# Kernel tuning notes

Measured on AMD Instinct MI355X. Metric: run time of the kernel, lower is better.

Reference implementation:

```python
import jax, jax.numpy as jnp
import numpy as np

B, C, H, W = 2, 512, 32, 32
HEADS = 8      # attention heads
GROUPS = 8     # offset groups (defaults to heads)
DH = 64        # dim_head
DF = 4         # downsample_factor
OFF_SCALE = 4.0
EPS = 1e-5


def _bn(t, gamma, beta):
    # eval-mode BatchNorm2d with running_mean=0, running_var=1
    s = gamma / jnp.sqrt(1.0 + EPS)
    return t * s[None, :, None, None] + beta[None, :, None, None]


def _gconv1x1(t, w):
    # grouped 1x1 conv (bias-free); w: (GROUPS, out_per_group, in_per_group)
    b, c, h, ww = t.shape
    o = jnp.einsum('bgci,goc->bgoi', t.reshape(b, GROUPS, c // GROUPS, h * ww), w)
    return o.reshape(b, GROUPS * w.shape[1], h, ww)


def _grid_sample(img, grid):
    # F.grid_sample: bilinear, padding_mode='zeros', align_corners=False
    # img: (N,Ci,Hi,Wi); grid: (N,Hg,Wg,2), grid[...,0]=x, grid[...,1]=y in [-1,1]
    N, Ci, Hi, Wi = img.shape
    gx = (grid[..., 0] + 1.0) * (Wi / 2.0) - 0.5
    gy = (grid[..., 1] + 1.0) * (Hi / 2.0) - 0.5
    x0 = jnp.floor(gx)
    y0 = jnp.floor(gy)
    wx = gx - x0
    wy = gy - y0

    def gather(im, ix, iy):
        valid = (ix >= 0) & (ix < Wi) & (iy >= 0) & (iy < Hi)
        ixc = jnp.clip(ix, 0, Wi - 1).astype(jnp.int32)
        iyc = jnp.clip(iy, 0, Hi - 1).astype(jnp.int32)
        return im[:, iyc, ixc] * valid[None].astype(im.dtype)

    def sample_one(im, x0, y0, wx, wy):
        v00 = gather(im, x0, y0)
        v01 = gather(im, x0 + 1, y0)
        v10 = gather(im, x0, y0 + 1)
        v11 = gather(im, x0 + 1, y0 + 1)
        wx = wx[None]
        wy = wy[None]
        return (v00 * (1 - wx) * (1 - wy) + v01 * wx * (1 - wy)
                + v10 * (1 - wx) * wy + v11 * wx * wy)

    return jax.vmap(sample_one)(img, x0, y0, wx, wy)


def _forward(x, bn1_g, bn1_b, bn2_g, bn2_b, qw, kw, vw, out_w, out_b,
             off_dw_w, off_dw_b, off_pw_w,
             cpb_w1, cpb_b1, cpb_w2, cpb_b2, cpb_w3, cpb_b3,
             mlp_w1, mlp_b1, mlp_w2, mlp_b2):
    b = x.shape[0]
    xn = _bn(x, bn1_g, bn1_b)
    # ---- deformable attention ----
    q = _gconv1x1(xn, qw)                                   # (b, 512, H, W)
    qg = q.reshape(b * GROUPS, DH, H, W)
    # to_offsets: depthwise conv k=6, s=4, p=1 -> GELU -> 1x1(64->2) -> tanh * offset_scale
    off = jax.lax.conv_general_dilated(
        qg, off_dw_w, (DF, DF), ((1, 1), (1, 1)),
        dimension_numbers=('NCHW', 'OIHW', 'NCHW'), feature_group_count=DH)
    off = jax.nn.gelu(off + off_dw_b[None, :, None, None], approximate=False)
    off = jnp.tanh(jnp.einsum('bchw,oc->bohw', off, off_pw_w)) * OFF_SCALE   # (b*G, 2, Hd, Wd)
    Hd, Wd = off.shape[-2], off.shape[-1]
    gy, gx = jnp.meshgrid(jnp.arange(Hd, dtype=x.dtype), jnp.arange(Wd, dtype=x.dtype), indexing='ij')
    vx = gx[None] + off[:, 0]
    vy = gy[None] + off[:, 1]
    # normalize_grid (lucidrains): first comp by (Hd-1), second by (Wd-1)
    nx = 2.0 * vx / max(Hd - 1, 1) - 1.0
    ny = 2.0 * vy / max(Wd - 1, 1) - 1.0
    vgrid_scaled = jnp.stack((nx, ny), axis=-1)             # (b*G, Hd, Wd, 2)
    kv = _grid_sample(xn.reshape(b * GROUPS, DH, H, W), vgrid_scaled)
    kv = kv.reshape(b, GROUPS * DH, Hd, Wd)
    k = _gconv1x1(kv, kw)
    v = _gconv1x1(kv, vw)
    scale = DH ** -0.5
    qh = q.reshape(b, HEADS, DH, H * W).transpose(0, 1, 3, 2) * scale    # (b,h,i,d)
    kh = k.reshape(b, HEADS, DH, Hd * Wd).transpose(0, 1, 3, 2)          # (b,h,j,d)
    vh = v.reshape(b, HEADS, DH, Hd * Wd).transpose(0, 1, 3, 2)
    # continuous relative position bias (CPB)
    qgy, qgx = jnp.meshgrid(jnp.arange(H, dtype=x.dtype), jnp.arange(W, dtype=x.dtype), indexing='ij')
    grid_q = jnp.stack((2.0 * qgx / max(H - 1, 1) - 1.0,
                        2.0 * qgy / max(W - 1, 1) - 1.0), axis=-1).reshape(1, H * W, 2)
    grid_kv = vgrid_scaled.reshape(b * GROUPS, Hd * Wd, 2)
    pos = grid_q[:, :, None, :] - grid_kv[:, None, :, :]    # (b*G, i, j, 2)
    bias = jnp.sign(pos) * jnp.log1p(jnp.abs(pos))
    bias = jax.nn.relu(bias @ cpb_w1 + cpb_b1)
    bias = jax.nn.relu(bias @ cpb_w2 + cpb_b2)
    bias = (bias @ cpb_w3 + cpb_b3).reshape(b, GROUPS, H * W, Hd * Wd)   # heads//groups == 1
    sim = jnp.einsum('bhid,bhjd->bhij', qh, kh) + bias
    attn = jax.nn.softmax(sim, axis=-1)
    out = jnp.einsum('bhij,bhjd->bhid', attn, vh)
    out = out.transpose(0, 1, 3, 2).reshape(b, HEADS * DH, H, W)
    out = jnp.einsum('bchw,oc->bohw', out, out_w) + out_b[None, :, None, None]
    x = x + out
    # ---- conv1x1 MLP ----
    xn2 = _bn(x, bn2_g, bn2_b)
    h1 = jax.nn.gelu(jnp.einsum('bchw,oc->bohw', xn2, mlp_w1) + mlp_b1[None, :, None, None],
                     approximate=False)
    return x + jnp.einsum('bchw,oc->bohw', h1, mlp_w2) + mlp_b2[None, :, None, None]


def setup_inputs():
    ks = jax.random.split(jax.random.key(0), 16)
    w = lambda k, shape: jax.random.normal(k, shape, dtype=jnp.float32) * 0.02
    return {
        'x': jax.random.normal(ks[0], (B, C, H, W), dtype=jnp.float32),
        'bn1_g': jnp.ones((C,), jnp.float32),
        'bn1_b': jnp.zeros((C,), jnp.float32),
        'bn2_g': jnp.ones((C,), jnp.float32),
        'bn2_b': jnp.zeros((C,), jnp.float32),
        'qw': w(ks[1], (GROUPS, DH, C // GROUPS)),
        'kw': w(ks[2], (GROUPS, DH, C // GROUPS)),
        'vw': w(ks[3], (GROUPS, DH, C // GROUPS)),
        'out_w': w(ks[4], (C, HEADS * DH)),
        'out_b': jnp.zeros((C,), jnp.float32),
        'off_dw_w': w(ks[5], (DH, 1, 6, 6)),
        'off_dw_b': jnp.zeros((DH,), jnp.float32),
        'off_pw_w': w(ks[6], (2, DH)),
        'cpb_w1': w(ks[7], (2, 128)),
        'cpb_b1': jnp.zeros((128,), jnp.float32),
        'cpb_w2': w(ks[8], (128, 128)),
        'cpb_b2': jnp.zeros((128,), jnp.float32),
        'cpb_w3': w(ks[9], (128, 1)),
        'cpb_b3': jnp.zeros((1,), jnp.float32),
        'mlp_w1': w(ks[10], (4 * C, C)),
        'mlp_b1': jnp.zeros((4 * C,), jnp.float32),
        'mlp_w2': w(ks[11], (C, 4 * C)),
        'mlp_b2': jnp.zeros((C,), jnp.float32),
    }


def reference(x, bn1_g, bn1_b, bn2_g, bn2_b, qw, kw, vw, out_w, out_b,
              off_dw_w, off_dw_b, off_pw_w,
              cpb_w1, cpb_b1, cpb_w2, cpb_b2, cpb_w3, cpb_b3,
              mlp_w1, mlp_b1, mlp_w2, mlp_b2):
    return _forward(x, bn1_g, bn1_b, bn2_g, bn2_b, qw, kw, vw, out_w, out_b,
                    off_dw_w, off_dw_b, off_pw_w,
                    cpb_w1, cpb_b1, cpb_w2, cpb_b2, cpb_w3, cpb_b3,
                    mlp_w1, mlp_b1, mlp_w2, mlp_b2)
```

## Files before the change

kernel.cpp:

```cpp
#include <hip/hip_runtime.h>
#include <hip/hip_bf16.h>
#include <math.h>

#define BB 2
#define CC 512
#define HH 32
#define WW 32
#define HWP 1024
#define GG 8
#define DH 64
#define HD 8
#define WD 8
#define JJ 64
#define BG 16
#define EPS 1e-5f

typedef __attribute__((ext_vector_type(8))) short short8;
typedef __attribute__((ext_vector_type(4))) short s16x4;
typedef __attribute__((ext_vector_type(4))) float f32x4;
typedef __attribute__((ext_vector_type(4))) unsigned short u16x4;
typedef __attribute__((ext_vector_type(4))) unsigned int u32x4;

static __device__ __forceinline__ short f2bf(float x) {
    unsigned u = __builtin_bit_cast(unsigned, x);
    u += 0x7FFFu + ((u >> 16) & 1u);
    return (short)(u >> 16);
}
static __device__ __forceinline__ float bf2f(unsigned short h) {
    return __builtin_bit_cast(float, (unsigned)h << 16);
}

__global__ void k_wpack(const float* __restrict__ qw, const float* __restrict__ ow,
                        const float* __restrict__ w1, const float* __restrict__ w2,
                        const float* __restrict__ cw2, const float* __restrict__ kw,
                        const float* __restrict__ vw, const float* __restrict__ dww,
                        unsigned short* __restrict__ wp, unsigned short* __restrict__ w2p,
                        float* __restrict__ kwt, float* __restrict__ vwt,
                        float* __restrict__ dwt) {
    int idx = blockIdx.x * 256 + threadIdx.x;
    if (idx < 2392064) {
        float v;
        if (idx < 32768) v = qw[idx];
        else if (idx < 294912) v = ow[idx - 32768];
        else if (idx < 1343488) v = w1[idx - 294912];
        else v = w2[idx - 1343488];
        wp[idx] = (unsigned short)f2bf(v);
    } else if (idx < 2408448) {
        int i2 = idx - 2392064;
        int k = i2 >> 7, n = i2 & 127;
        int dest = ((((n >> 4) * 4 + (k >> 5)) * 64) + (((k >> 3) & 3) * 16) + (n & 15)) * 8 + (k & 7);
        w2p[dest] = (unsigned short)f2bf(cw2[i2]);
    } else if (idx < 2441216) {
        int i2 = idx - 2408448;
        int o = i2 & 63, c = (i2 >> 6) & 63, g = i2 >> 12;
        kwt[i2] = kw[(size_t)(g * 64 + o) * 64 + c];
    } else if (idx < 2473984) {
        int i2 = idx - 2441216;
        int o = i2 & 63, c = (i2 >> 6) & 63, g = i2 >> 12;
        vwt[i2] = vw[(size_t)(g * 64 + o) * 64 + c];
    } else if (idx < 2476288) {
        int i2 = idx - 2473984;
        int ch = i2 & 63, k = i2 >> 6;
        dwt[i2] = dww[ch * 36 + k];
    }
}

__global__ __launch_bounds__(256) void k_qgemm(
    const float* __restrict__ x, const float* __restrict__ g1,
    const float* __restrict__ b1, const unsigned short* __restrict__ qwp,
    unsigned short* __restrict__ qt) {
    __shared__ __align__(16) short As[64][72];
    __shared__ __align__(16) short Bs[64][72];
    int blk = blockIdx.x;
    int bg = blk >> 4, nt = blk & 15;
    int b = bg >> 3, g = bg & 7;
    int i0 = nt * 64;
    int tid = threadIdx.x, lane = tid & 63, wv = tid >> 6;
    int wm = (wv >> 1) * 32, wn = (wv & 1) * 32;
    int l15 = lane & 15, quad = lane >> 4;
    const float invs = 1.0f / sqrtf(1.0f + EPS);
    {
        int c4 = (tid & 15) * 4;
        int ob = tid >> 4;
#pragma unroll
        for (int p = 0; p < 4; p++) {
            int o = ob + p * 16;
            u16x4 v = *(const u16x4*)(qwp + (size_t)(g * 64 + o) * 64 + c4);
            *(u16x4*)&As[o][c4] = v;
        }
    }
    {
        int i4 = (tid & 15) * 4;
        int cb = tid >> 4;
#pragma unroll
        for (int p = 0; p < 4; p++) {
            int c = cb + p * 16;
            f32x4 v = *(const f32x4*)(x + (size_t)(b * CC + g * 64 + c) * HWP + i0 + i4);
            float sc = g1[g * 64 + c] * invs;
            float sh = b1[g * 64 + c];
            Bs[i4 + 0][c] = f2bf(fmaf(v.x, sc, sh));
            Bs[i4 + 1][c] = f2bf(fmaf(v.y, sc, sh));
            Bs[i4 + 2][c] = f2bf(fmaf(v.z, sc, sh));
            Bs[i4 + 3][c] = f2bf(fmaf(v.w, sc, sh));
        }
    }
    __syncthreads();
    f32x4 acc[2][2];
#pragma unroll
    for (int a = 0; a < 2; a++)
#pragma unroll
        for (int c = 0; c < 2; c++) acc[a][c] = (f32x4){0.f, 0.f, 0.f, 0.f};
#pragma unroll
    for (int ks = 0; ks < 2; ks++) {
        short8 af0 = *(const short8*)&As[wm + l15][ks * 32 + quad * 8];
        short8 af1 = *(const short8*)&As[wm + 16 + l15][ks * 32 + quad * 8];
        short8 bf0 = *(const short8*)&Bs[wn + l15][ks * 32 + quad * 8];
        short8 bf1 = *(const short8*)&Bs[wn + 16 + l15][ks * 32 + quad * 8];
        acc[0][0] = __builtin_amdgcn_mfma_f32_16x16x32_bf16(af0, bf0, acc[0][0], 0, 0, 0);
        acc[0][1] = __builtin_amdgcn_mfma_f32_16x16x32_bf16(af0, bf1, acc[0][1], 0, 0, 0);
        acc[1][0] = __builtin_amdgcn_mfma_f32_16x16x32_bf16(af1, bf0, acc[1][0], 0, 0, 0);
        acc[1][1] = __builtin_amdgcn_mfma_f32_16x16x32_bf16(af1, bf1, acc[1][1], 0, 0, 0);
    }
    __syncthreads();
#pragma unroll
    for (int im = 0; im < 2; im++)
#pragma unroll
        for (int r = 0; r < 4; r++) {
            int m = wm + im * 16 + quad * 4 + r;
#pragma unroll
            for (int in_ = 0; in_ < 2; in_++) {
                int n = wn + in_ * 16 + l15;
                As[n][m] = f2bf(acc[im][in_][r]);
            }
        }
    __syncthreads();
    {
        int n = tid >> 2;
        int c0 = (tid & 3) * 16;
        short8 a = *(const short8*)&As[n][c0];
        short8 c = *(const short8*)&As[n][c0 + 8];
        unsigned short* dst = qt + ((size_t)bg * 1024 + i0 + n) * 64 + c0;
        *(short8*)dst = a;
        *(short8*)(dst + 8) = c;
    }
}

__global__ __launch_bounds__(64) void k_offskv(
    const unsigned short* __restrict__ qt, const float* __restrict__ dwt,
    const float* __restrict__ dwb, const float* __restrict__ pw,
    const float* __restrict__ x, const float* __restrict__ g1,
    const float* __restrict__ b1, const float* __restrict__ kwt,
    const float* __restrict__ vwt, float* __restrict__ vgrid,
    unsigned short* __restrict__ kkh, unsigned short* __restrict__ vvh) {
    __shared__ float sm[64];
    int blk = blockIdx.x;
    int bg = blk >> 6;
    int hd = (blk >> 3) & 7;
    int wd = blk & 7;
    int g = bg & 7, b = bg >> 3;
    int ch = threadIdx.x;
    const unsigned short* qb = qt + (size_t)bg * 65536;
    float acc = 0.f;
#pragma unroll
    for (int kh = 0; kh < 6; kh++) {
        int hin = hd * 4 - 1 + kh;
        if (hin < 0 || hin >= HH) continue;
#pragma unroll
        for (int kw_ = 0; kw_ < 6; kw_++) {
            int win = wd * 4 - 1 + kw_;
            if (win < 0 || win >= WW) continue;
            acc = fmaf(bf2f(qb[(hin * WW + win) * 64 + ch]),
                       dwt[(kh * 6 + kw_) * 64 + ch], acc);
        }
    }
    acc += dwb[ch];
    float ge = 0.5f * acc * (1.0f + erff(acc * 0.7071067811865475f));
    float p0 = ge * pw[ch];
    float p1 = ge * pw[64 + ch];
#pragma unroll
    for (int off = 32; off; off >>= 1) {
        p0 += __shfl_xor(p0, off);
        p1 += __shfl_xor(p1, off);
    }
    float nx = 2.0f * ((float)wd + tanhf(p0) * 4.0f) / 7.0f - 1.0f;
    float ny = 2.0f * ((float)hd + tanhf(p1) * 4.0f) / 7.0f - 1.0f;
    if (ch == 0) {
        vgrid[blk * 2] = nx;
        vgrid[blk * 2 + 1] = ny;
    }
    {
        int cg = g * 64 + ch;
        const float invs = 1.0f / sqrtf(1.0f + EPS);
        float s = g1[cg] * invs;
        float bv = b1[cg];
        float gx = (nx + 1.0f) * 16.0f - 0.5f;
        float gy = (ny + 1.0f) * 16.0f - 0.5f;
        float x0f = floorf(gx), y0f = floorf(gy);
        float wx = gx - x0f, wy = gy - y0f;
        int x0 = (int)x0f, y0 = (int)y0f;
        const float* im = x + (size_t)(b * CC + cg) * HWP;
        float sx = 0.f, sw = 0.f;
        float w00 = (1 - wx) * (1 - wy), w01 = wx * (1 - wy);
        float w10 = (1 - wx) * wy, w11 = wx * wy;
        if (x0 >= 0 && x0 < WW && y0 >= 0 && y0 < HH)                 { sx += w00 * im[y0 * WW + x0];           sw += w00; }
        if (x0 + 1 >= 0 && x0 + 1 < WW && y0 >= 0 && y0 < HH)         { sx += w01 * im[y0 * WW + x0 + 1];       sw += w01; }
        if (x0 >= 0 && x0 < WW && y0 + 1 >= 0 && y0 + 1 < HH)         { sx += w10 * im[(y0 + 1) * WW + x0];     sw += w10; }
        if (x0 + 1 >= 0 && x0 + 1 < WW && y0 + 1 >= 0 && y0 + 1 < HH) { sx += w11 * im[(y0 + 1) * WW + x0 + 1]; sw += w11; }
        sm[ch] = s * sx + bv * sw;
    }
    __syncthreads();
    int j = blk & 63;
    const float* kwr = kwt + g * 4096 + ch;
    const float* vwr = vwt + g * 4096 + ch;
    float ak = 0.f, av = 0.f;
#pragma unroll
    for (int c = 0; c < 64; c++) {
        float tv = sm[c];
        ak = fmaf(tv, kwr[c * 64], ak);
        av = fmaf(tv, vwr[c * 64], av);
    }
    kkh[(size_t)bg * 4096 + j * 64 + ch] = (unsigned short)f2bf(ak);
    vvh[(size_t)bg * 4096 + j * 64 + ch] = (unsigned short)f2bf(av);
}

__global__ __launch_bounds__(256) void k_cpb(
    const float* __restrict__ vgrid, const unsigned short* __restrict__ w2p,
    const float* __restrict__ w1, const float* __restrict__ b1,
    const float* __restrict__ b2, const float* __restrict__ w3,
    const float* __restrict__ b3, unsigned short* __restrict__ bias) {
    __shared__ __align__(16) short w2fs[16384];
    int tid = threadIdx.x;
    {
        const u32x4* src = (const u32x4*)w2p;
        u32x4* dst = (u32x4*)w2fs;
        for (int c = tid; c < 2048; c += 256) dst[c] = src[c];
    }
    float bias3 = b3[0];
    __syncthreads();

    int lane = tid & 63;
    int wv = tid >> 6;
    int l15 = lane & 15;
    int quad = lane >> 4;

#pragma unroll 1
    for (int it = 0; it < 4; it++) {
        int p = (blockIdx.x * 4 + it) * 4 + wv;
        int pu = __builtin_amdgcn_readfirstlane(p);
        int cofs = (int)((unsigned)pu >> 20);
        int bg = p >> 11;
        int i = (p >> 1) & 1023;
        int jbase = (p & 1) * 32;
        int hi = i >> 5, wi = i & 31;
        float qx = 2.0f * (float)wi / 31.0f - 1.0f;
        float qy = 2.0f * (float)hi / 31.0f - 1.0f;

        int jA = jbase + l15;
        float gkxA = vgrid[(bg * 64 + jA) * 2];
        float gkyA = vgrid[(bg * 64 + jA) * 2 + 1];
        float gkxB = vgrid[(bg * 64 + jA + 16) * 2];
        float gkyB = vgrid[(bg * 64 + jA + 16) * 2 + 1];
        float p0 = qx - gkxA, p1 = qy - gkyA;
        float s0a = copysignf(log1pf(fabsf(p0)), p0);
        float s1a = copysignf(log1pf(fabsf(p1)), p1);
        p0 = qx - gkxB; p1 = qy - gkyB;
        float s0b = copysignf(log1pf(fabsf(p0)), p0);
        float s1b = copysignf(log1pf(fabsf(p1)), p1);

        short8 hA[4], hB[4];
#pragma unroll
        for (int kc = 0; kc < 4; kc++) {
            f32x4 cu0 = *(const f32x4*)(w1 + cofs + kc * 32 + quad * 8);
            f32x4 cu1 = *(const f32x4*)(w1 + cofs + kc * 32 + quad * 8 + 4);
            f32x4 cv0 = *(const f32x4*)(w1 + cofs + 128 + kc * 32 + quad * 8);
            f32x4 cv1 = *(const f32x4*)(w1 + cofs + 128 + kc * 32 + quad * 8 + 4);
            f32x4 cb0 = *(const f32x4*)(b1 + cofs + kc * 32 + quad * 8);
            f32x4 cb1 = *(const f32x4*)(b1 + cofs + kc * 32 + quad * 8 + 4);
            u32x4 pa, pb;
#pragma unroll
            for (int j2 = 0; j2 < 4; j2++) {
                int e0 = 2 * j2, e1 = 2 * j2 + 1;
                float u0 = (e0 < 4) ? cu0[e0] : cu1[e0 - 4];
                float u1 = (e1 < 4) ? cu0[e1] : cu1[e1 - 4];
                float v0 = (e0 < 4) ? cv0[e0] : cv1[e0 - 4];
                float v1 = (e1 < 4) ? cv0[e1] : cv1[e1 - 4];
                float c0 = (e0 < 4) ? cb0[e0] : cb1[e0 - 4];
                float c1 = (e1 < 4) ? cb0[e1] : cb1[e1 - 4];
                unsigned a0 = __builtin_bit_cast(unsigned,
                    fmaxf(fmaf(s0a, u0, fmaf(s1a, v0, c0)), 0.f)) + 0x8000u;
                unsigned a1 = __builtin_bit_cast(unsigned,
                    fmaxf(fmaf(s0a, u1, fmaf(s1a, v1, c1)), 0.f)) + 0x8000u;
                pa[j2] = __builtin_amdgcn_perm(a1, a0, 0x07060302);
                unsigned b0 = __builtin_bit_cast(unsigned,
                    fmaxf(fmaf(s0b, u0, fmaf(s1b, v0, c0)), 0.f)) + 0x8000u;
                unsigned b1_ = __builtin_bit_cast(unsigned,
                    fmaxf(fmaf(s0b, u1, fmaf(s1b, v1, c1)), 0.f)) + 0x8000u;
                pb[j2] = __builtin_amdgcn_perm(b1_, b0, 0x07060302);
            }
            hA[kc] = __builtin_bit_cast(short8, pa);
            hB[kc] = __builtin_bit_cast(short8, pb);
        }

        float psumA = 0.f, psumB = 0.f;
#pragma unroll 2
        for (int nt = 0; nt < 8; nt++) {
            f32x4 accA = (f32x4){0.f, 0.f, 0.f, 0.f};
            f32x4 accB = (f32x4){0.f, 0.f, 0.f, 0.f};
#pragma unroll
            for (int kc = 0; kc < 4; kc++) {
                short8 af = *(const short8*)(w2fs + (((nt * 4 + kc) * 64) + lane) * 8);
                accA = __builtin_amdgcn_mfma_f32_16x16x32_bf16(af, hA[kc], accA, 0, 0, 0);
                accB = __builtin_amdgcn_mfma_f32_16x16x32_bf16(af, hB[kc], accB, 0, 0, 0);
            }
            f32x4 b2q = *(const f32x4*)(b2 + cofs + nt * 16 + quad * 4);
            f32x4 w3q = *(const f32x4*)(w3 + cofs + nt * 16 + quad * 4);
#pragma unroll
            for (int r = 0; r < 4; r++) {
                psumA = fmaf(fmaxf(accA[r] + b2q[r], 0.f), w3q[r], psumA);
                psumB = fmaf(fmaxf(accB[r] + b2q[r], 0.f), w3q[r], psumB);
            }
        }
        psumA += __shfl_xor(psumA, 16);
        psumA += __shfl_xor(psumA, 32);
        psumB += __shfl_xor(psumB, 16);
        psumB += __shfl_xor(psumB, 32);
        if (quad == 0) {
            bias[(size_t)(p * 2 + 0) * 16 + l15] = (unsigned short)f2bf(psumA + bias3);
            bias[(size_t)(p * 2 + 1) * 16 + l15] = (unsigned short)f2bf(psumB + bias3);
        }
    }
}

__global__ __launch_bounds__(256) void k_attn(
    const unsigned short* __restrict__ qt, const unsigned short* __restrict__ kkh,
    const unsigned short* __restrict__ vvh, const unsigned short* __restrict__ bias,
    unsigned short* __restrict__ ao) {
    __shared__ __align__(16) short Ks[64][72];
    __shared__ __align__(16) short Vt[64][72];
    __shared__ __align__(16) short Qs[64][72];
    __shared__ __align__(16) short Ps[4][16][72];
    int blk = blockIdx.x;
    int bg = blk >> 4;
    int chunk = blk & 15;
    int i0 = chunk * 64;
    int b = bg >> 3, g = bg & 7;
    int tid = threadIdx.x, lane = tid & 63, wv = tid >> 6;
    int l15 = lane & 15, quad = lane >> 4;

    const unsigned short* kbase = kkh + (size_t)bg * 4096;
    const unsigned short* vbase = vvh + (size_t)bg * 4096;
#pragma unroll
    for (int it = 0; it < 2; it++) {
        int e8 = (it * 256 + tid) * 8;
        int j = e8 >> 6, d = e8 & 63;
        u32x4 v = *(const u32x4*)(kbase + e8);
        *(u32x4*)&Ks[j][d] = v;
    }
    if (tid < 128) {
        int d0 = (tid & 15) * 4;
        int jb = (tid >> 4) * 8;
        u16x4 rb[8];
#pragma unroll
        for (int p = 0; p < 8; p++)
            rb[p] = *(const u16x4*)(vbase + (jb + p) * 64 + d0);
#pragma unroll
        for (int q = 0; q < 4; q++) {
            u32x4 w;
#pragma unroll
            for (int jj = 0; jj < 4; jj++) {
                unsigned lo = ((const unsigned*)&rb[2 * jj])[q >> 1];
                unsigned hi = ((const unsigned*)&rb[2 * jj + 1])[q >> 1];
                w[jj] = (q & 1) ? __builtin_amdgcn_perm(hi, lo, 0x07060302)
                                : __builtin_amdgcn_perm(hi, lo, 0x05040100);
            }
            *(u32x4*)&Vt[d0 + q][jb] = w;
        }
    }
    {
        const unsigned short* qtb = qt + ((size_t)bg * 1024 + i0) * 64;
#pragma unroll
        for (int it = 0; it < 4; it++) {
            int e4 = it * 1024 + tid * 4;
            int i = e4 >> 6, d = e4 & 63;
            u16x4 v = *(const u16x4*)(qtb + e4);
            *(u16x4*)&Qs[i][d] = v;
        }
    }
    __syncthreads();

    int iw = wv * 16;
    f32x4 Sacc[4];
#pragma unroll
    for (int nt = 0; nt < 4; nt++) Sacc[nt] = (f32x4){0.f, 0.f, 0.f, 0.f};
#pragma unroll
    for (int ks = 0; ks < 2; ks++) {
        short8 aq = *(const short8*)&Qs[iw + l15][quad * 8 + ks * 32];
#pragma unroll
        for (int nt = 0; nt < 4; nt++) {
            short8 bk = *(const short8*)&Ks[nt * 16 + l15][quad * 8 + ks * 32];
            Sacc[nt] = __builtin_amdgcn_mfma_f32_16x16x32_bf16(aq, bk, Sacc[nt], 0, 0, 0);
        }
    }
    const unsigned short* bp = bias + ((size_t)bg * 1024 + i0 + iw + quad * 4) * 64 + l15;
    float Sv[4][4];
#pragma unroll
    for (int nt = 0; nt < 4; nt++)
#pragma unroll
        for (int r = 0; r < 4; r++)
            Sv[nt][r] = fmaf(Sacc[nt][r], 0.125f, bf2f(bp[r * 64 + nt * 16]));
#pragma unroll
    for (int r = 0; r < 4; r++) {
        float m = fmaxf(fmaxf(Sv[0][r], Sv[1][r]), fmaxf(Sv[2][r], Sv[3][r]));
        m = fmaxf(m, __shfl_xor(m, 1));
        m = fmaxf(m, __shfl_xor(m, 2));
        m = fmaxf(m, __shfl_xor(m, 4));
        m = fmaxf(m, __shfl_xor(m, 8));
        float l = 0.f;
#pragma unroll
        for (int nt = 0; nt < 4; nt++) { Sv[nt][r] = expf(Sv[nt][r] - m); l += Sv[nt][r]; }
        l += __shfl_xor(l, 1);
        l += __shfl_xor(l, 2);
        l += __shfl_xor(l, 4);
        l += __shfl_xor(l, 8);
        float inv = 1.0f / l;
#pragma unroll
        for (int nt = 0; nt < 4; nt++)
            Ps[wv][quad * 4 + r][nt * 16 + l15] = f2bf(Sv[nt][r] * inv);
    }
    f32x4 Oacc[4];
#pragma unroll
    for (int nt = 0; nt < 4; nt++) Oacc[nt] = (f32x4){0.f, 0.f, 0.f, 0.f};
#pragma unroll
    for (int ks = 0; ks < 2; ks++) {
        short8 ap = *(const short8*)&Ps[wv][l15][quad * 8 + ks * 32];
#pragma unroll
        for (int nt = 0; nt < 4; nt++) {
            short8 bv = *(const short8*)&Vt[nt * 16 + l15][quad * 8 + ks * 32];
            Oacc[nt] = __builtin_amdgcn_mfma_f32_16x16x32_bf16(ap, bv, Oacc[nt], 0, 0, 0);
        }
    }
    __syncthreads();
#pragma unroll
    for (int nt = 0; nt < 4; nt++) {
        s16x4 o4 = {f2bf(Oacc[nt][0]), f2bf(Oacc[nt][1]), f2bf(Oacc[nt][2]), f2bf(Oacc[nt][3])};
        *(s16x4*)&Qs[nt * 16 + l15][iw + quad * 4] = o4;
    }
    __syncthreads();
    {
        int d = tid >> 2;
        int ic = (tid & 3) * 16;
        short8 a = *(const short8*)&Qs[d][ic];
        short8 c = *(const short8*)&Qs[d][ic + 8];
        unsigned short* dst = ao + (size_t)(b * CC + g * 64 + d) * HWP + i0 + ic;
        *(short8*)dst = a;
        *(short8*)(dst + 8) = c;
    }
}

template<int EPI, int KD, int BK, int MT>
__global__ __launch_bounds__(256) void k_gemm(
    const unsigned short* __restrict__ A, const unsigned short* __restrict__ Bh,
    const float* __restrict__ resid, const float* __restrict__ bias,
    void* __restrict__ outp, unsigned short* __restrict__ out2,
    const float* __restrict__ bns, const float* __restrict__ bnb) {
    constexpr int MM = MT * 64;
    constexpr int KV4 = BK / 4;
    constexpr int RP = 256 / KV4;
    constexpr int NA = 64 / RP;
    constexpr int NB = BK / 16;
    __shared__ __align__(16) short As[64][BK + 8];
    __shared__ __align__(16) short Bs[64][BK + 8];
    int tid = threadIdx.x;
    int blk = blockIdx.x;
    int mt = blk & (MT - 1);
    int nb = blk / MT;
    int bb = nb >> 4, nt = nb & 15;
    int m0 = mt * 64, i0 = nt * 64;
    int lane = tid & 63, wv = tid >> 6;
    int wm = (wv >> 1) * 32, wn = (wv & 1) * 32;
    int l15 = lane & 15, quad = lane >> 4;
    const unsigned short* Af = A + (size_t)m0 * KD;
    const float invs = 1.0f / sqrtf(1.0f + EPS);
    int kk4 = (tid & (KV4 - 1)) * 4;
    int myb = tid / KV4;
    int i4 = (tid & 15) * 4;
    int kyb8 = (tid >> 4) * NB;

    f32x4 acc[2][2];
#pragma unroll
    for (int a = 0; a < 2; a++)
#pragma unroll
        for (int c = 0; c < 2; c++) acc[a][c] = (f32x4){0.f, 0.f, 0.f, 0.f};

    u16x4 ra[NA], rb[NB];
#pragma unroll
    for (int p = 0; p < NA; p++)
        ra[p] = *(const u16x4*)(Af + (size_t)(myb + p * RP) * KD + kk4);
#pragma unroll
    for (int p = 0; p < NB; p++)
        rb[p] = *(const u16x4*)(Bh + (size_t)bb * KD * HWP + (size_t)(kyb8 + p) * HWP + i0 + i4);

    for (int k0 = 0; k0 < KD; k0 += BK) {
        __syncthreads();
#pragma unroll
        for (int p = 0; p < NA; p++)
            *(u16x4*)&As[myb + p * RP][kk4] = ra[p];
#pragma unroll
        for (int q = 0; q < 4; q++) {
            u32x4 w;
#pragma unroll
            for (int j = 0; j < 4; j++) {
                unsigned lo = ((const unsigned*)&rb[2 * j])[q >> 1];
                unsigned hi = ((const unsigned*)&rb[2 * j + 1])[q >> 1];
                w[j] = (q & 1) ? __builtin_amdgcn_perm(hi, lo, 0x07060302)
                               : __builtin_amdgcn_perm(hi, lo, 0x05040100);
            }
            *(u32x4*)&Bs[i4 + q][kyb8] = w;
        }
        __syncthreads();
        int kn = k0 + BK;
        if (kn < KD) {
#pragma unroll
            for (int p = 0; p < NA; p++)
                ra[p] = *(const u16x4*)(Af + (size_t)(myb + p * RP) * KD + kn + kk4);
#pragma unroll
            for (int p = 0; p < NB; p++)
                rb[p] = *(const u16x4*)(Bh + (size_t)bb * KD * HWP + (size_t)(kn + kyb8 + p) * HWP + i0 + i4);
        }
#pragma unroll
        for (int ks = 0; ks < BK / 32; ks++) {
            short8 af0 = *(const short8*)&As[wm + l15][ks * 32 + quad * 8];
            short8 af1 = *(const short8*)&As[wm + 16 + l15][ks * 32 + quad * 8];
            short8 bf0 = *(const short8*)&Bs[wn + l15][ks * 32 + quad * 8];
            short8 bf1 = *(const short8*)&Bs[wn + 16 + l15][ks * 32 + quad * 8];
            acc[0][0] = __builtin_amdgcn_mfma_f32_16x16x32_bf16(af0, bf0, acc[0][0], 0, 0, 0);
            acc[0][1] = __builtin_amdgcn_mfma_f32_16x16x32_bf16(af0, bf1, acc[0][1], 0, 0, 0);
            acc[1][0] = __builtin_amdgcn_mfma_f32_16x16x32_bf16(af1, bf0, acc[1][0], 0, 0, 0);
            acc[1][1] = __builtin_amdgcn_mfma_f32_16x16x32_bf16(af1, bf1, acc[1][1], 0, 0, 0);
        }
    }

    float* outF = (float*)outp;
    unsigned short* outH = (unsigned short*)outp;
#pragma unroll
    for (int im = 0; im < 2; im++) {
#pragma unroll
        for (int r = 0; r < 4; r++) {
            int m = m0 + wm + im * 16 + quad * 4 + r;
            float bv = bias[m];
#pragma unroll
            for (int in_ = 0; in_ < 2; in_++) {
                int n = i0 + wn + in_ * 16 + l15;
                size_t idx = ((size_t)bb * MM + m) * HWP + n;
                float v = acc[im][in_][r] + bv;
                if constexpr (EPI == 1) {
                    float ge = 0.5f * v * (1.0f + erff(v * 0.7071067811865475f));
                    outH[idx] = (unsigned short)f2bf(ge);
                } else if constexpr (EPI == 3) {
                    float vr = v + resid[idx];
                    outF[idx] = vr;
                    out2[idx] = (unsigned short)f2bf(fmaf(vr, bns[m] * invs, bnb[m]));
                } else {
                    outF[idx] = v + resid[idx];
                }
            }
        }
    }
}

extern "C" void kernel_launch(void* const* d_in, const int* in_sizes, int n_in,
                              void* d_out, int out_size, void* d_ws, size_t ws_size,
                              hipStream_t stream) {
    const float* x      = (const float*)d_in[0];
    const float* bn1_g  = (const float*)d_in[1];
    const float* bn1_b  = (const float*)d_in[2];
    const float* bn2_g  = (const float*)d_in[3];
    const float* bn2_b  = (const float*)d_in[4];
    const float* qw     = (const float*)d_in[5];
    const float* kw     = (const float*)d_in[6];
    const float* vw     = (const float*)d_in[7];
    const float* out_w  = (const float*)d_in[8];
    const float* out_b  = (const float*)d_in[9];
    const float* off_dw_w = (const float*)d_in[10];
    const float* off_dw_b = (const float*)d_in[11];
    const float* off_pw_w = (const float*)d_in[12];
    const float* cpb_w1 = (const float*)d_in[13];
    const float* cpb_b1 = (const float*)d_in[14];
    const float* cpb_w2 = (const float*)d_in[15];
    const float* cpb_b2 = (const float*)d_in[16];
    const float* cpb_w3 = (const float*)d_in[17];
    const float* cpb_b3 = (const float*)d_in[18];
    const float* mlp_w1 = (const float*)d_in[19];
    const float* mlp_b1 = (const float*)d_in[20];
    const float* mlp_w2 = (const float*)d_in[21];
    const float* mlp_b2 = (const float*)d_in[22];

    float* ws = (float*)d_ws;
    unsigned short* qt = (unsigned short*)(ws + 1048576);
    float* vgrid = ws + 2097152;
    unsigned short* kkh = (unsigned short*)(ws + 2164736);
    unsigned short* vvh = (unsigned short*)(ws + 2230272);
    unsigned short* w2p = (unsigned short*)(ws + 2295808);
    unsigned short* ao  = (unsigned short*)(ws + 2312192);
    unsigned short* xn2 = (unsigned short*)(ws + 2836480);
    float* xo    = ws + 3360768;
    float* h1of  = ws + 4409344;
    unsigned short* biasb = (unsigned short*)h1of;
    unsigned short* h1o = (unsigned short*)h1of;
    unsigned short* wp  = (unsigned short*)(ws + 6506496);
    unsigned short* qwp  = wp;
    unsigned short* owp  = wp + 32768;
    unsigned short* w1p  = wp + 294912;
    unsigned short* w2mp = wp + 1343488;
    float* kwt = ws + 7702528;
    float* vwt = ws + 7735296;
    float* dwt = ws + 7768064;

    hipLaunchKernelGGL(k_wpack, dim3(9673), dim3(256), 0, stream,
                       qw, out_w, mlp_w1, mlp_w2, cpb_w2, kw, vw, off_dw_w,
                       wp, w2p, kwt, vwt, dwt);
    hipLaunchKernelGGL(k_qgemm, dim3(256), dim3(256), 0, stream, x, bn1_g, bn1_b, qwp, qt);
    hipLaunchKernelGGL(k_offskv, dim3(1024), dim3(64), 0, stream,
                       qt, dwt, off_dw_b, off_pw_w, x, bn1_g, bn1_b, kwt, vwt,
                       vgrid, kkh, vvh);
    hipLaunchKernelGGL(k_cpb, dim3(2048), dim3(256), 0, stream,
                       vgrid, w2p, cpb_w1, cpb_b1, cpb_b2, cpb_w3, cpb_b3, biasb);
    hipLaunchKernelGGL(k_attn, dim3(256), dim3(256), 0, stream, qt, kkh, vvh, biasb, ao);
    k_gemm<3, 512, 128, 8><<<dim3(256), dim3(256), 0, stream>>>(
        owp, ao, x, out_b, xo, xn2, bn2_g, bn2_b);
    k_gemm<1, 512, 128, 32><<<dim3(1024), dim3(256), 0, stream>>>(
        w1p, xn2, nullptr, mlp_b1, h1o, nullptr, nullptr, nullptr);
    k_gemm<2, 2048, 128, 8><<<dim3(256), dim3(256), 0, stream>>>(
        w2mp, h1o, xo, mlp_b2, d_out, nullptr, nullptr, nullptr);
}
```

Measured before the change: 234.2 us.

## Store bf16 GEMM intermediates pixel-major to drop in-kernel B transposes

The attention output and the bf16 GEMM outputs (normalized residual and GELU hidden) are now written in pixel-major [b][pixel][channel] layout, staged through shared memory so the global stores are coalesced. The GEMM's B operand can then be loaded with the same contiguous-K pattern as A. This removes the perm-based register transpose when filling the B tile. In exchange the epilogue gains an extra LDS round trip and barrier, and LDS writes with a strided column pattern may bank-conflict.

```diff
diff --git a/kernel.cpp b/kernel.cpp
--- a/kernel.cpp
+++ b/kernel.cpp
@@ -441,17 +441,17 @@
     }
     __syncthreads();
 #pragma unroll
-    for (int nt = 0; nt < 4; nt++) {
-        s16x4 o4 = {f2bf(Oacc[nt][0]), f2bf(Oacc[nt][1]), f2bf(Oacc[nt][2]), f2bf(Oacc[nt][3])};
-        *(s16x4*)&Qs[nt * 16 + l15][iw + quad * 4] = o4;
-    }
+    for (int nt = 0; nt < 4; nt++)
+#pragma unroll
+        for (int r = 0; r < 4; r++)
+            Qs[iw + quad * 4 + r][nt * 16 + l15] = f2bf(Oacc[nt][r]);
     __syncthreads();
     {
-        int d = tid >> 2;
-        int ic = (tid & 3) * 16;
-        short8 a = *(const short8*)&Qs[d][ic];
-        short8 c = *(const short8*)&Qs[d][ic + 8];
-        unsigned short* dst = ao + (size_t)(b * CC + g * 64 + d) * HWP + i0 + ic;
+        int il = tid >> 2;
+        int c0 = (tid & 3) * 16;
+        short8 a = *(const short8*)&Qs[il][c0];
+        short8 c = *(const short8*)&Qs[il][c0 + 8];
+        unsigned short* dst = ao + ((size_t)b * 1024 + i0 + il) * 512 + g * 64 + c0;
         *(short8*)dst = a;
         *(short8*)(dst + 8) = c;
     }
@@ -459,7 +459,7 @@
 
 template<int EPI, int KD, int BK, int MT>
 __global__ __launch_bounds__(256) void k_gemm(
-    const unsigned short* __restrict__ A, const unsigned short* __restrict__ Bh,
+    const unsigned short* __restrict__ A, const unsigned short* __restrict__ Bt,
     const float* __restrict__ resid, const float* __restrict__ bias,
     void* __restrict__ outp, unsigned short* __restrict__ out2,
     const float* __restrict__ bns, const float* __restrict__ bnb) {
@@ -467,7 +467,6 @@
     constexpr int KV4 = BK / 4;
     constexpr int RP = 256 / KV4;
     constexpr int NA = 64 / RP;
-    constexpr int NB = BK / 16;
     __shared__ __align__(16) short As[64][BK + 8];
     __shared__ __align__(16) short Bs[64][BK + 8];
     int tid = threadIdx.x;
@@ -480,11 +479,10 @@
     int wm = (wv >> 1) * 32, wn = (wv & 1) * 32;
     int l15 = lane & 15, quad = lane >> 4;
     const unsigned short* Af = A + (size_t)m0 * KD;
+    const unsigned short* Bf = Bt + ((size_t)bb * HWP + i0) * KD;
     const float invs = 1.0f / sqrtf(1.0f + EPS);
     int kk4 = (tid & (KV4 - 1)) * 4;
     int myb = tid / KV4;
-    int i4 = (tid & 15) * 4;
-    int kyb8 = (tid >> 4) * NB;
 
     f32x4 acc[2][2];
 #pragma unroll
@@ -492,40 +490,28 @@
 #pragma unroll
         for (int c = 0; c < 2; c++) acc[a][c] = (f32x4){0.f, 0.f, 0.f, 0.f};
 
-    u16x4 ra[NA], rb[NB];
-#pragma unroll
-    for (int p = 0; p < NA; p++)
+    u16x4 ra[NA], rb[NA];
+#pragma unroll
+    for (int p = 0; p < NA; p++) {
         ra[p] = *(const u16x4*)(Af + (size_t)(myb + p * RP) * KD + kk4);
-#pragma unroll
-    for (int p = 0; p < NB; p++)
-        rb[p] = *(const u16x4*)(Bh + (size_t)bb * KD * HWP + (size_t)(kyb8 + p) * HWP + i0 + i4);
+        rb[p] = *(const u16x4*)(Bf + (size_t)(myb + p * RP) * KD + kk4);
+    }
 
     for (int k0 = 0; k0 < KD; k0 += BK) {
         __syncthreads();
 #pragma unroll
-        for (int p = 0; p < NA; p++)
+        for (int p = 0; p < NA; p++) {
             *(u16x4*)&As[myb + p * RP][kk4] = ra[p];
-#pragma unroll
-        for (int q = 0; q < 4; q++) {
-            u32x4 w;
-#pragma unroll
-            for (int j = 0; j < 4; j++) {
-                unsigned lo = ((const unsigned*)&rb[2 * j])[q >> 1];
-                unsigned hi = ((const unsigned*)&rb[2 * j + 1])[q >> 1];
-                w[j] = (q & 1) ? __builtin_amdgcn_perm(hi, lo, 0x07060302)
-                               : __builtin_amdgcn_perm(hi, lo, 0x05040100);
-            }
-            *(u32x4*)&Bs[i4 + q][kyb8] = w;
+            *(u16x4*)&Bs[myb + p * RP][kk4] = rb[p];
         }
         __syncthreads();
         int kn = k0 + BK;
         if (kn < KD) {
 #pragma unroll
-            for (int p = 0; p < NA; p++)
+            for (int p = 0; p < NA; p++) {
                 ra[p] = *(const u16x4*)(Af + (size_t)(myb + p * RP) * KD + kn + kk4);
-#pragma unroll
-            for (int p = 0; p < NB; p++)
-                rb[p] = *(const u16x4*)(Bh + (size_t)bb * KD * HWP + (size_t)(kn + kyb8 + p) * HWP + i0 + i4);
+                rb[p] = *(const u16x4*)(Bf + (size_t)(myb + p * RP) * KD + kn + kk4);
+            }
         }
 #pragma unroll
         for (int ks = 0; ks < BK / 32; ks++) {
@@ -541,30 +527,42 @@
     }
 
     float* outF = (float*)outp;
-    unsigned short* outH = (unsigned short*)outp;
+    if constexpr (EPI == 1 || EPI == 3) __syncthreads();
 #pragma unroll
     for (int im = 0; im < 2; im++) {
 #pragma unroll
         for (int r = 0; r < 4; r++) {
             int m = m0 + wm + im * 16 + quad * 4 + r;
+            int ml = wm + im * 16 + quad * 4 + r;
             float bv = bias[m];
 #pragma unroll
             for (int in_ = 0; in_ < 2; in_++) {
-                int n = i0 + wn + in_ * 16 + l15;
+                int nl = wn + in_ * 16 + l15;
+                int n = i0 + nl;
                 size_t idx = ((size_t)bb * MM + m) * HWP + n;
                 float v = acc[im][in_][r] + bv;
                 if constexpr (EPI == 1) {
                     float ge = 0.5f * v * (1.0f + erff(v * 0.7071067811865475f));
-                    outH[idx] = (unsigned short)f2bf(ge);
+                    As[nl][ml] = f2bf(ge);
                 } else if constexpr (EPI == 3) {
                     float vr = v + resid[idx];
                     outF[idx] = vr;
-                    out2[idx] = (unsigned short)f2bf(fmaf(vr, bns[m] * invs, bnb[m]));
+                    As[nl][ml] = f2bf(fmaf(vr, bns[m] * invs, bnb[m]));
                 } else {
                     outF[idx] = v + resid[idx];
                 }
             }
         }
+    }
+    if constexpr (EPI == 1 || EPI == 3) {
+        __syncthreads();
+        int il = tid >> 2;
+        int c0 = (tid & 3) * 16;
+        short8 a = *(const short8*)&As[il][c0];
+        short8 c = *(const short8*)&As[il][c0 + 8];
+        unsigned short* dst = out2 + ((size_t)bb * HWP + i0 + il) * MM + m0 + c0;
+        *(short8*)dst = a;
+        *(short8*)(dst + 8) = c;
     }
 }
 
@@ -629,7 +627,7 @@
     k_gemm<3, 512, 128, 8><<<dim3(256), dim3(256), 0, stream>>>(
         owp, ao, x, out_b, xo, xn2, bn2_g, bn2_b);
     k_gemm<1, 512, 128, 32><<<dim3(1024), dim3(256), 0, stream>>>(
-        w1p, xn2, nullptr, mlp_b1, h1o, nullptr, nullptr, nullptr);
+        w1p, xn2, nullptr, mlp_b1, nullptr, h1o, nullptr, nullptr);
     k_gemm<2, 2048, 128, 8><<<dim3(256), dim3(256), 0, stream>>>(
         w2mp, h1o, xo, mlp_b2, d_out, nullptr, nullptr, nullptr);
 }
```

Result: faster. 228.1 us, median of 2 (-2.6%).
